# Kernel tuning notes

Hardware: AMD Instinct MI355X
Metric: run time of the kernel (lower is better)

The kernel has to match this reference:

```python
import jax, jax.numpy as jnp
import numpy as np

D_MODEL = 1024
H = 16
D_K = D_MODEL // H
D_FF = 4096
EPS = 1e-6
NEG = -1.0e9


def setup_inputs() -> dict:
    key = jax.random.key(0)
    ks = jax.random.split(key, 8)
    B, S = 4, 2048
    x = jax.random.normal(ks[0], (B, S, D_MODEL), dtype=jnp.float32)
    src_mask = jnp.ones((B, 1, S, S), dtype=jnp.int32)
    s = 0.02
    wq = jax.random.normal(ks[1], (D_MODEL, D_MODEL), jnp.float32) * s
    wk = jax.random.normal(ks[2], (D_MODEL, D_MODEL), jnp.float32) * s
    wv = jax.random.normal(ks[3], (D_MODEL, D_MODEL), jnp.float32) * s
    wo = jax.random.normal(ks[4], (D_MODEL, D_MODEL), jnp.float32) * s
    w1 = jax.random.normal(ks[5], (D_MODEL, D_FF), jnp.float32) * s
    b1 = jnp.zeros((D_FF,), jnp.float32)
    w2 = jax.random.normal(ks[6], (D_FF, D_MODEL), jnp.float32) * s
    b2 = jnp.zeros((D_MODEL,), jnp.float32)
    # LayerNorm params are scalars in the original (torch.ones(1)/zeros(1))
    a1 = jnp.ones((1,), jnp.float32); bt1 = jnp.zeros((1,), jnp.float32)
    a2 = jnp.ones((1,), jnp.float32); bt2 = jnp.zeros((1,), jnp.float32)
    return {"x": x, "src_mask": src_mask, "wq": wq, "wk": wk, "wv": wv,
            "wo": wo, "w1": w1, "b1": b1, "w2": w2, "b2": b2,
            "a1": a1, "bt1": bt1, "a2": a2, "bt2": bt2}


def _layernorm(x, alpha, beta):
    # Original: (x - mean) / (std + eps), std with Bessel correction (torch default)
    mean = jnp.mean(x, axis=-1, keepdims=True)
    std = jnp.std(x, axis=-1, keepdims=True, ddof=1)
    return alpha * (x - mean) / (std + EPS) + beta


def _mha(x, mask, wq, wk, wv, wo):
    B, S, _ = x.shape
    q = (x @ wq).reshape(B, S, H, D_K).transpose(0, 2, 1, 3)  # [B,H,S,Dk]
    k = (x @ wk).reshape(B, S, H, D_K).transpose(0, 2, 1, 3)
    v = (x @ wv).reshape(B, S, H, D_K).transpose(0, 2, 1, 3)
    scores = jnp.einsum('bhqd,bhkd->bhqk', q, k) / jnp.sqrt(jnp.float32(D_K))
    scores = jnp.where(mask == 0, NEG, scores)
    attn = jax.nn.softmax(scores, axis=-1)
    out = jnp.einsum('bhqk,bhkd->bhqd', attn, v)  # [B,H,S,Dk]
    out = out.transpose(0, 2, 1, 3).reshape(B, S, D_MODEL)
    return out @ wo


def reference(x, src_mask, wq, wk, wv, wo, w1, b1, w2, b2, a1, bt1, a2, bt2):
    # Sublayer 1: self-attention with post-norm residual (dropout = eval/identity)
    attn_out = _mha(x, src_mask, wq, wk, wv, wo)
    x = _layernorm(x + attn_out, a1, bt1)
    # Sublayer 2: FFN with post-norm residual
    ffn_out = jax.nn.relu(x @ w1 + b1) @ w2 + b2
    x = _layernorm(x + ffn_out, a2, bt2)
    return x
```

## Files before the change

kernel.cpp:

```cpp
#include <hip/hip_runtime.h>
#include <stdint.h>

typedef __bf16 bf16x8 __attribute__((ext_vector_type(8)));
typedef float f32x4 __attribute__((ext_vector_type(4)));
typedef unsigned short u16;
typedef u16 u16x8 __attribute__((ext_vector_type(8)));
typedef u16 u16x4 __attribute__((ext_vector_type(4)));
typedef uint32_t u32;

#define DEV __device__ __forceinline__

static constexpr int B_ = 4, S_ = 2048, M_ = 8192, D_ = 1024, H_ = 16, DFF_ = 4096;

DEV u16 f2bf(float f) {
    union { float f; u32 u; } c; c.f = f;
    u32 u = c.u;
    return (u16)((u + 0x7fffu + ((u >> 16) & 1u)) >> 16);
}

DEV u32 cvt_pk_bf16(float lo, float hi) {
    u32 r;
    asm("v_cvt_pk_bf16_f32 %0, %1, %2" : "=v"(r) : "v"(lo), "v"(hi));
    return r;
}

DEV float v_exp2(float x) {
    float r;
    asm("v_exp_f32 %0, %1" : "=v"(r) : "v"(x));
    return r;
}

DEV void gload16(void* lds, const void* g) {
    __builtin_amdgcn_global_load_lds(
        (const __attribute__((address_space(1))) unsigned int*)g,
        (__attribute__((address_space(3))) unsigned int*)lds, 16, 0, 0);
}


__global__ __launch_bounds__(256) void k_pack_mask(const int* __restrict__ m,
                                                   u32* __restrict__ bits, int nwords) {
    int w = blockIdx.x * 256 + threadIdx.x;
    if (w >= nwords) return;
    const int4* s = (const int4*)(m + (size_t)w * 32);
    u32 r = 0;
#pragma unroll
    for (int j = 0; j < 8; j++) {
        int4 v = s[j];
        r |= (u32)(v.x != 0) << (j * 4) | (u32)(v.y != 0) << (j * 4 + 1) |
             (u32)(v.z != 0) << (j * 4 + 2) | (u32)(v.w != 0) << (j * 4 + 3);
    }
    bits[w] = r;
}

__global__ __launch_bounds__(256) void k_cast_bf16(const float* __restrict__ s,
                                                   u16* __restrict__ d, int n4) {
    int i = blockIdx.x * 256 + threadIdx.x;
    if (i >= n4) return;
    f32x4 v = ((const f32x4*)s)[i];
    u16x4 o;
    o[0] = f2bf(v[0]); o[1] = f2bf(v[1]); o[2] = f2bf(v[2]); o[3] = f2bf(v[3]);
    ((u16x4*)d)[i] = o;
}

__global__ void k_transpose_cast(const float* __restrict__ s, u16* __restrict__ d,
                                 int K, int N) {
    __shared__ float t[32][33];
    int n0 = blockIdx.x * 32, k0 = blockIdx.y * 32;
    int tx = threadIdx.x, ty = threadIdx.y;
#pragma unroll
    for (int i = 0; i < 4; i++)
        t[ty + i * 8][tx] = s[(size_t)(k0 + ty + i * 8) * N + n0 + tx];
    __syncthreads();
#pragma unroll
    for (int i = 0; i < 4; i++)
        d[(size_t)(n0 + ty + i * 8) * K + k0 + tx] = f2bf(t[tx][ty + i * 8]);
}

__global__ __launch_bounds__(256) void k_transpose_v(const u16* __restrict__ qkv,
                                                     u16* __restrict__ vT) {
    __shared__ u16 t[64][68];
    const int bh = blockIdx.y, s0 = blockIdx.x * 64;
    const int r = threadIdx.x >> 2, c = (threadIdx.x & 3) * 16;
    const u16* src = qkv + ((size_t)(128 + bh) * 2048 + s0 + r) * 64 + c;
    *(u16x8*)&t[r][c] = *(const u16x8*)src;
    *(u16x8*)&t[r][c + 8] = *(const u16x8*)(src + 8);
    __syncthreads();
    u16x8 o0, o1;
#pragma unroll
    for (int e = 0; e < 8; e++) { o0[e] = t[c + e][r]; o1[e] = t[c + 8 + e][r]; }
    u16* dst = vT + ((size_t)bh * 64 + r) * 2048 + s0 + c;
    *(u16x8*)dst = o0;
    *(u16x8*)(dst + 8) = o1;
}

template <int EPI>
__global__ __launch_bounds__(512, 4) void k_gemm8(const u16* __restrict__ A,
                                                  const u16* __restrict__ Bt,
                                                  float* __restrict__ Cf,
                                                  u16* __restrict__ Cb,
                                                  const float* __restrict__ bias,
                                                  int N, int K) {
    __shared__ u16 As[2][128 * 64];
    __shared__ u16 Bs[2][128 * 64];
    const int tid = threadIdx.x, lane = tid & 63, wave = tid >> 6;
    const int lr = lane & 15, lg = lane >> 4;
    const int wm = wave >> 1, wn = wave & 1;
    const int nbx = N >> 7;
    const int chunk = gridDim.x >> 3;
    const int id = ((int)blockIdx.x & 7) * chunk + ((int)blockIdx.x >> 3);
    const size_t row0 = (size_t)(id / nbx) * 128;
    const int col0 = (id % nbx) * 128;
    const int srow = lane >> 3;
    const int sgr = (lane & 7) ^ (srow & 7);
    const int NT = K >> 6;
    f32x4 acc[2][4] = {};

    auto stage = [&](int buf, int t) {
#pragma unroll
        for (int i = 0; i < 2; i++) {
            int c = i * 8 + wave;
            gload16((char*)&As[buf][0] + c * 1024,
                    (const char*)(A + (row0 + c * 8 + srow) * K + t * 64 + sgr * 8));
        }
#pragma unroll
        for (int i = 0; i < 2; i++) {
            int c = i * 8 + wave;
            gload16((char*)&Bs[buf][0] + c * 1024,
                    (const char*)(Bt + (size_t)(col0 + c * 8 + srow) * K + t * 64 + sgr * 8));
        }
    };

    stage(0, 0);
    for (int t = 0; t < NT; ++t) {
        const int cur = t & 1;
        if (t + 1 < NT) {
            stage(cur ^ 1, t + 1);
            asm volatile("s_waitcnt vmcnt(4)" ::: "memory");
        } else {
            asm volatile("s_waitcnt vmcnt(0)" ::: "memory");
        }
        __builtin_amdgcn_s_barrier();
        asm volatile("" ::: "memory");
        bf16x8 bF[4][2];
#pragma unroll
        for (int n = 0; n < 4; n++) {
            int r = wn * 64 + n * 16 + lr;
            int rb = r * 128, sw = (r & 7) << 4;
#pragma unroll
            for (int ks = 0; ks < 2; ks++)
                bF[n][ks] = *(const bf16x8*)((char*)&Bs[cur][0] +
                                             (rb + ((ks * 64 + lg * 16) ^ sw)));
        }
#pragma unroll
        for (int m = 0; m < 2; m++) {
            int r = wm * 32 + m * 16 + lr;
            int rb = r * 128, sw = (r & 7) << 4;
            bf16x8 a0 = *(const bf16x8*)((char*)&As[cur][0] + (rb + ((lg * 16) ^ sw)));
            bf16x8 a1 = *(const bf16x8*)((char*)&As[cur][0] + (rb + ((64 + lg * 16) ^ sw)));
            __builtin_amdgcn_s_setprio(1);
#pragma unroll
            for (int n = 0; n < 4; n++) {
                acc[m][n] = __builtin_amdgcn_mfma_f32_16x16x32_bf16(a0, bF[n][0],
                                                                    acc[m][n], 0, 0, 0);
                acc[m][n] = __builtin_amdgcn_mfma_f32_16x16x32_bf16(a1, bF[n][1],
                                                                    acc[m][n], 0, 0, 0);
            }
            __builtin_amdgcn_s_setprio(0);
        }
        asm volatile("" ::: "memory");
        __builtin_amdgcn_s_barrier();
    }
#pragma unroll
    for (int m = 0; m < 2; m++)
#pragma unroll
        for (int n = 0; n < 4; n++)
#pragma unroll
            for (int i = 0; i < 4; i++) {
                int rg = (int)row0 + wm * 32 + m * 16 + lg * 4 + i;
                int cg = col0 + wn * 64 + n * 16 + lr;
                float v = acc[m][n][i];
                if constexpr (EPI == 0) {
                    if (cg < 1024) v *= 0.1803368801111832f;
                    int proj = cg >> 10, hh = (cg >> 6) & 15, dk = cg & 63;
                    int b = rg >> 11, s = rg & 2047;
                    size_t idx = ((size_t)(proj * 64 + b * 16 + hh) * 2048 + s) * 64 + dk;
                    Cb[idx] = f2bf(v);
                } else if constexpr (EPI == 1) {
                    Cf[(size_t)rg * N + cg] = v;
                } else if constexpr (EPI == 2) {
                    v += bias[cg];
                    v = v > 0.f ? v : 0.f;
                    Cb[(size_t)rg * N + cg] = f2bf(v);
                } else {
                    Cf[(size_t)rg * N + cg] = v + bias[cg];
                }
            }
}

__global__ __launch_bounds__(256) void k_attn(const u16* __restrict__ qkv,
                                              const u16* __restrict__ vT,
                                              const u32* __restrict__ mbits,
                                              u16* __restrict__ outb) {
    __shared__ u16 Kt[64 * 64];
    __shared__ u16 Vt[64 * 64];
    __shared__ u16 Pt[4][32 * 64];
    __shared__ u32 pm[128][2];
    const int tid = threadIdx.x, lane = tid & 63, wave = tid >> 6;
    const int lr = lane & 15, lg = lane >> 4;
    const int id0 = blockIdx.y * 16 + blockIdx.x;
    const int id = (id0 & 7) * 128 + (id0 >> 3);
    const int bh = id >> 4;
    const int b = bh >> 4, h = bh & 15;
    const int qb0 = (id & 15) * 128;
    const size_t qbase = (size_t)bh * (2048 * 64);
    const size_t kbase = (size_t)(64 + bh) * (2048 * 64);
    const size_t vtbase = (size_t)bh * (64 * 2048);

    bf16x8 qf[2][2];
    const int q0 = qb0 + wave * 32;
#pragma unroll
    for (int rs = 0; rs < 2; rs++)
#pragma unroll
        for (int kf = 0; kf < 2; kf++)
            qf[rs][kf] = *(const bf16x8*)(qkv + qbase +
                                          (size_t)(q0 + rs * 16 + lr) * 64 + kf * 32 + lg * 8);

    u16x8 ones_u;
#pragma unroll
    for (int e = 0; e < 8; e++) ones_u[e] = 0x3f80;
    const bf16x8 ones8 = *(const bf16x8*)&ones_u;

    f32x4 o[2][4] = {};
    f32x4 lacc[2] = {};
    const int str = tid >> 2, sq = tid & 3;
    const int swzs = (str & 7) << 4;
    const f32x4 zinit = {-16.f, -16.f, -16.f, -16.f};

    for (int kv0 = 0; kv0 < 2048; kv0 += 64) {
        __syncthreads();
        {
            const u16* src = qkv + kbase + (size_t)(kv0 + str) * 64 + sq * 16;
            u16x8 v0 = *(const u16x8*)src, v1 = *(const u16x8*)(src + 8);
            int b0 = str * 128 + sq * 32;
            *(u16x8*)((char*)Kt + ((b0) ^ swzs)) = v0;
            *(u16x8*)((char*)Kt + ((b0 + 16) ^ swzs)) = v1;
        }
        {
            const u16* src = vT + vtbase + (size_t)str * 2048 + kv0 + sq * 16;
            u16x8 v0 = *(const u16x8*)src, v1 = *(const u16x8*)(src + 8);
            int b0 = str * 128 + sq * 32;
            *(u16x8*)((char*)Vt + ((b0) ^ swzs)) = v0;
            *(u16x8*)((char*)Vt + ((b0 + 16) ^ swzs)) = v1;
        }
        int ql = tid >> 1, wsel = tid & 1;
        u32 mword = mbits[(size_t)(b * 2048 + qb0 + ql) * 64 + (kv0 >> 5) + wsel];
        pm[ql][wsel] = mword;
        bool allones = (__ballot(mword == 0xffffffffu) == ~0ull);
        __syncthreads();

        f32x4 st[2][4];
#pragma unroll
        for (int ks = 0; ks < 4; ks++) {
            int rr = ks * 16 + lr;
            int rb = rr * 128, sw = (rr & 7) << 4;
            bf16x8 k0 = *(const bf16x8*)((char*)Kt + ((rb + lg * 16) ^ sw));
            bf16x8 k1 = *(const bf16x8*)((char*)Kt + ((rb + 64 + lg * 16) ^ sw));
#pragma unroll
            for (int rs = 0; rs < 2; rs++) {
                f32x4 z = __builtin_amdgcn_mfma_f32_16x16x32_bf16(k0, qf[rs][0],
                                                                  zinit, 0, 0, 0);
                z = __builtin_amdgcn_mfma_f32_16x16x32_bf16(k1, qf[rs][1], z, 0, 0, 0);
                st[rs][ks] = z;
            }
        }
        if (!allones) {
#pragma unroll
            for (int rs = 0; rs < 2; rs++) {
                u32 w0 = pm[wave * 32 + rs * 16 + lr][0];
                u32 w1 = pm[wave * 32 + rs * 16 + lr][1];
#pragma unroll
                for (int ks = 0; ks < 4; ks++)
#pragma unroll
                    for (int i = 0; i < 4; i++) {
                        int kv = ks * 16 + lg * 4 + i;
                        u32 w = (kv & 32) ? w1 : w0;
                        if (!((w >> (kv & 31)) & 1u)) st[rs][ks][i] = -1e9f;
                    }
            }
        }
#pragma unroll
        for (int rs = 0; rs < 2; rs++) {
            int prow = rs * 16 + lr;
            int pb = prow * 128, swp = (prow & 7) << 4;
#pragma unroll
            for (int ks = 0; ks < 4; ks++) {
                uint2 w;
                w.x = cvt_pk_bf16(v_exp2(st[rs][ks][0]), v_exp2(st[rs][ks][1]));
                w.y = cvt_pk_bf16(v_exp2(st[rs][ks][2]), v_exp2(st[rs][ks][3]));
                *(uint2*)((char*)&Pt[wave][0] + ((pb + ks * 32 + lg * 8) ^ swp)) = w;
            }
        }
        asm volatile("s_waitcnt lgkmcnt(0)" ::: "memory");
        bf16x8 pf[2][2];
#pragma unroll
        for (int rs = 0; rs < 2; rs++) {
            int prow = rs * 16 + lr;
            int pb = prow * 128, swp = (prow & 7) << 4;
            pf[rs][0] = *(const bf16x8*)((char*)&Pt[wave][0] + ((pb + lg * 16) ^ swp));
            pf[rs][1] = *(const bf16x8*)((char*)&Pt[wave][0] + ((pb + 64 + lg * 16) ^ swp));
        }
#pragma unroll
        for (int rs = 0; rs < 2; rs++) {
            lacc[rs] = __builtin_amdgcn_mfma_f32_16x16x32_bf16(ones8, pf[rs][0],
                                                               lacc[rs], 0, 0, 0);
            lacc[rs] = __builtin_amdgcn_mfma_f32_16x16x32_bf16(ones8, pf[rs][1],
                                                               lacc[rs], 0, 0, 0);
        }
#pragma unroll
        for (int ns = 0; ns < 4; ns++) {
            int vr = ns * 16 + lr;
            int vb = vr * 128, sw = (vr & 7) << 4;
            bf16x8 v0 = *(const bf16x8*)((char*)Vt + ((vb + lg * 16) ^ sw));
            bf16x8 v1 = *(const bf16x8*)((char*)Vt + ((vb + 64 + lg * 16) ^ sw));
#pragma unroll
            for (int rs = 0; rs < 2; rs++) {
                o[rs][ns] = __builtin_amdgcn_mfma_f32_16x16x32_bf16(v0, pf[rs][0],
                                                                    o[rs][ns], 0, 0, 0);
                o[rs][ns] = __builtin_amdgcn_mfma_f32_16x16x32_bf16(v1, pf[rs][1],
                                                                    o[rs][ns], 0, 0, 0);
            }
        }
    }
#pragma unroll
    for (int rs = 0; rs < 2; rs++) {
        float inv = 1.f / lacc[rs][0];
        int qg = qb0 + wave * 32 + rs * 16 + lr;
#pragma unroll
        for (int ns = 0; ns < 4; ns++) {
            u16x4 ov;
#pragma unroll
            for (int i = 0; i < 4; i++) ov[i] = f2bf(o[rs][ns][i] * inv);
            *(u16x4*)(outb + (size_t)(b * 2048 + qg) * 1024 + h * 64 + ns * 16 + lg * 4) = ov;
        }
    }
}

template <bool WB>
__global__ __launch_bounds__(256) void k_add_ln(const float* __restrict__ y,
                                                const float* __restrict__ resid,
                                                float* __restrict__ outf,
                                                u16* __restrict__ outb,
                                                const float* __restrict__ alpha,
                                                const float* __restrict__ beta) {
    const int row = blockIdx.x, tid = threadIdx.x;
    const f32x4 a = ((const f32x4*)(y + (size_t)row * 1024))[tid];
    const f32x4 r = ((const f32x4*)(resid + (size_t)row * 1024))[tid];
    f32x4 t;
#pragma unroll
    for (int i = 0; i < 4; i++) t[i] = a[i] + r[i];
    float s = t[0] + t[1] + t[2] + t[3];
    float ss = t[0] * t[0] + t[1] * t[1] + t[2] * t[2] + t[3] * t[3];
#pragma unroll
    for (int m2 = 1; m2 < 64; m2 <<= 1) {
        s += __shfl_xor(s, m2);
        ss += __shfl_xor(ss, m2);
    }
    __shared__ float ps[4], pss[4];
    if ((tid & 63) == 0) { ps[tid >> 6] = s; pss[tid >> 6] = ss; }
    __syncthreads();
    s = ps[0] + ps[1] + ps[2] + ps[3];
    ss = pss[0] + pss[1] + pss[2] + pss[3];
    const float mean = s * (1.f / 1024.f);
    float var = (ss - 1024.f * mean * mean) * (1.f / 1023.f);
    var = fmaxf(var, 0.f);
    const float inv = alpha[0] / (sqrtf(var) + 1e-6f);
    const float bet = beta[0];
    f32x4 oo;
#pragma unroll
    for (int i = 0; i < 4; i++) oo[i] = (t[i] - mean) * inv + bet;
    ((f32x4*)(outf + (size_t)row * 1024))[tid] = oo;
    if constexpr (WB) {
        u16x4 ob;
#pragma unroll
        for (int i = 0; i < 4; i++) ob[i] = f2bf(oo[i]);
        ((u16x4*)(outb + (size_t)row * 1024))[tid] = ob;
    }
}

extern "C" void kernel_launch(void* const* d_in, const int* in_sizes, int n_in,
                              void* d_out, int out_size, void* d_ws, size_t ws_size,
                              hipStream_t stream) {
    const float* x   = (const float*)d_in[0];
    const int*   msk = (const int*)d_in[1];
    const float* wq  = (const float*)d_in[2];
    const float* wk  = (const float*)d_in[3];
    const float* wv  = (const float*)d_in[4];
    const float* wo  = (const float*)d_in[5];
    const float* w1  = (const float*)d_in[6];
    const float* b1  = (const float*)d_in[7];
    const float* w2  = (const float*)d_in[8];
    const float* b2  = (const float*)d_in[9];
    const float* a1  = (const float*)d_in[10];
    const float* bt1 = (const float*)d_in[11];
    const float* a2  = (const float*)d_in[12];
    const float* bt2 = (const float*)d_in[13];
    float* out = (float*)d_out;

    char* ws = (char*)d_ws;
    size_t off = 0;
    auto alloc = [&](size_t bytes) {
        void* p = ws + off;
        off += (bytes + 255) & ~(size_t)255;
        return p;
    };
    u16* xb    = (u16*)alloc((size_t)M_ * D_ * 2);
    u16* wqkvT = (u16*)alloc((size_t)3 * D_ * D_ * 2);
    u16* woT   = (u16*)alloc((size_t)D_ * D_ * 2);
    u16* w1T   = (u16*)alloc((size_t)DFF_ * D_ * 2);
    u16* w2T   = (u16*)alloc((size_t)D_ * DFF_ * 2);
    u32* mbits = (u32*)alloc((size_t)B_ * S_ * 64 * 4);
    u16* aout  = (u16*)alloc((size_t)M_ * D_ * 2);
    float* y   = (float*)alloc((size_t)M_ * D_ * 4);
    float* x1  = (float*)alloc((size_t)M_ * D_ * 4);
    u16* x1b   = (u16*)alloc((size_t)M_ * D_ * 2);
    u16* vTb   = (u16*)alloc((size_t)64 * 64 * 2048 * 2);
    u16* qkv   = (u16*)alloc((size_t)M_ * DFF_ * 2);
    u16* hft   = qkv;

    k_pack_mask<<<dim3((B_ * S_ * 64) / 256), 256, 0, stream>>>(msk, mbits, B_ * S_ * 64);
    k_cast_bf16<<<dim3((M_ * D_ / 4) / 256), 256, 0, stream>>>(x, xb, M_ * D_ / 4);
    dim3 tb(32, 8);
    k_transpose_cast<<<dim3(32, 32), tb, 0, stream>>>(wq, wqkvT, D_, D_);
    k_transpose_cast<<<dim3(32, 32), tb, 0, stream>>>(wk, wqkvT + D_ * D_, D_, D_);
    k_transpose_cast<<<dim3(32, 32), tb, 0, stream>>>(wv, wqkvT + 2 * D_ * D_, D_, D_);
    k_transpose_cast<<<dim3(32, 32), tb, 0, stream>>>(wo, woT, D_, D_);
    k_transpose_cast<<<dim3(128, 32), tb, 0, stream>>>(w1, w1T, D_, DFF_);
    k_transpose_cast<<<dim3(32, 128), tb, 0, stream>>>(w2, w2T, DFF_, D_);

    k_gemm8<0><<<dim3(1536), 512, 0, stream>>>(xb, wqkvT, nullptr, qkv, nullptr,
                                               3 * D_, D_);
    k_transpose_v<<<dim3(32, 64), 256, 0, stream>>>(qkv, vTb);
    k_attn<<<dim3(16, 64), 256, 0, stream>>>(qkv, vTb, mbits, aout);
    k_gemm8<1><<<dim3(512), 512, 0, stream>>>(aout, woT, y, nullptr, nullptr, D_, D_);
    k_add_ln<true><<<dim3(M_), 256, 0, stream>>>(y, x, x1, x1b, a1, bt1);
    k_gemm8<2><<<dim3(2048), 512, 0, stream>>>(x1b, w1T, nullptr, hft, b1, DFF_, D_);
    k_gemm8<3><<<dim3(512), 512, 0, stream>>>(hft, w2T, y, nullptr, b2, D_, DFF_);
    k_add_ln<false><<<dim3(M_), 256, 0, stream>>>(y, x1, out, nullptr, a2, bt2);
}
```

Baseline: 442.7 us.

## Add 256x256-tile pipelined GEMM for QKV/FFN1 and double-buffer attention K/V tiles

```diff
diff --git a/kernel.cpp b/kernel.cpp
--- a/kernel.cpp
+++ b/kernel.cpp
@@ -9,6 +9,7 @@
 typedef uint32_t u32;
 
 #define DEV __device__ __forceinline__
+#define MFMA(a, b, c) __builtin_amdgcn_mfma_f32_16x16x32_bf16(a, b, c, 0, 0, 0)
 
 static constexpr int B_ = 4, S_ = 2048, M_ = 8192, D_ = 1024, H_ = 16, DFF_ = 4096;
 
@@ -91,6 +92,153 @@
     u16* dst = vT + ((size_t)bh * 64 + r) * 2048 + s0 + c;
     *(u16x8*)dst = o0;
     *(u16x8*)(dst + 8) = o1;
+}
+
+template <int EPI>
+__global__ __launch_bounds__(512, 2) void k_gemm256(const u16* __restrict__ A,
+                                                    const u16* __restrict__ Bt,
+                                                    float* __restrict__ Cf,
+                                                    u16* __restrict__ Cb,
+                                                    const float* __restrict__ bias,
+                                                    int N, int K) {
+    __shared__ u16 As[2][256 * 64];
+    __shared__ u16 Bs[2][256 * 64];
+    const int tid = threadIdx.x, lane = tid & 63, wave = tid >> 6;
+    const int lr = lane & 15, lg = lane >> 4;
+    const int wm = wave >> 2, wn = wave & 3;
+    const int nbx = N >> 8;
+    const int chunk = gridDim.x >> 3;
+    const int id = ((int)blockIdx.x & 7) * chunk + ((int)blockIdx.x >> 3);
+    const size_t row0 = (size_t)(id / nbx) * 256;
+    const int col0 = (id % nbx) * 256;
+    const int srow = lane >> 3;
+    const int sgr = (lane & 7) ^ srow;
+    const int NT = K >> 6;
+    f32x4 acc[8][4] = {};
+
+    auto stage_half = [&](int isB, int buf, int t, int h) {
+        const u16* g = isB ? Bt : A;
+        const size_t grow0 = isB ? (size_t)col0 : row0;
+        char* base = isB ? (char*)&Bs[buf][0] : (char*)&As[buf][0];
+#pragma unroll
+        for (int l = 0; l < 2; l++) {
+            int rt = h * 128 + l * 64 + wave * 8;
+            gload16(base + rt * 128,
+                    (const char*)(g + (grow0 + rt + srow) * K + t * 64 + sgr * 8));
+        }
+    };
+    auto rdA = [&](int cur, int mh, int m, int kk) -> bf16x8 {
+        int r = wm * 128 + mh * 64 + m * 16 + lr;
+        int gi = kk * 4 + lg;
+        return *(const bf16x8*)((char*)&As[cur][0] + r * 128 + ((gi ^ (r & 7)) << 4));
+    };
+    auto rdB = [&](int cur, int nh, int n, int kk) -> bf16x8 {
+        int r = wn * 64 + nh * 32 + n * 16 + lr;
+        int gi = kk * 4 + lg;
+        return *(const bf16x8*)((char*)&Bs[cur][0] + r * 128 + ((gi ^ (r & 7)) << 4));
+    };
+
+    stage_half(0, 0, 0, 0); stage_half(0, 0, 0, 1);
+    stage_half(1, 0, 0, 0); stage_half(1, 0, 0, 1);
+    stage_half(1, 1, 1, 0); stage_half(1, 1, 1, 1);
+    asm volatile("s_waitcnt vmcnt(4)" ::: "memory");
+    __builtin_amdgcn_s_barrier();
+
+    bf16x8 aF[4][2], b0F[2][2], b1F[2][2];
+    for (int t = 0; t < NT; ++t) {
+        const int cur = t & 1, nxt = cur ^ 1;
+#pragma unroll
+        for (int m = 0; m < 4; m++) { aF[m][0] = rdA(cur, 0, m, 0); aF[m][1] = rdA(cur, 0, m, 1); }
+#pragma unroll
+        for (int n = 0; n < 2; n++) { b0F[n][0] = rdB(cur, 0, n, 0); b0F[n][1] = rdB(cur, 0, n, 1); }
+        if (t + 1 < NT) stage_half(0, nxt, t + 1, 0);
+        __builtin_amdgcn_s_barrier();
+        asm volatile("s_waitcnt lgkmcnt(0)" ::: "memory");
+        __builtin_amdgcn_sched_barrier(0);
+        __builtin_amdgcn_s_setprio(1);
+#pragma unroll
+        for (int m = 0; m < 4; m++)
+#pragma unroll
+            for (int n = 0; n < 2; n++) {
+                acc[m][n] = MFMA(aF[m][0], b0F[n][0], acc[m][n]);
+                acc[m][n] = MFMA(aF[m][1], b0F[n][1], acc[m][n]);
+            }
+        __builtin_amdgcn_s_setprio(0);
+        __builtin_amdgcn_s_barrier();
+#pragma unroll
+        for (int n = 0; n < 2; n++) { b1F[n][0] = rdB(cur, 1, n, 0); b1F[n][1] = rdB(cur, 1, n, 1); }
+        if (t + 1 < NT) stage_half(0, nxt, t + 1, 1);
+        __builtin_amdgcn_s_barrier();
+        asm volatile("s_waitcnt lgkmcnt(0)" ::: "memory");
+        __builtin_amdgcn_sched_barrier(0);
+        __builtin_amdgcn_s_setprio(1);
+#pragma unroll
+        for (int m = 0; m < 4; m++)
+#pragma unroll
+            for (int n = 0; n < 2; n++) {
+                acc[m][2 + n] = MFMA(aF[m][0], b1F[n][0], acc[m][2 + n]);
+                acc[m][2 + n] = MFMA(aF[m][1], b1F[n][1], acc[m][2 + n]);
+            }
+        __builtin_amdgcn_s_setprio(0);
+        __builtin_amdgcn_s_barrier();
+#pragma unroll
+        for (int m = 0; m < 4; m++) { aF[m][0] = rdA(cur, 1, m, 0); aF[m][1] = rdA(cur, 1, m, 1); }
+        if (t + 2 < NT) stage_half(1, cur, t + 2, 0);
+        __builtin_amdgcn_s_barrier();
+        asm volatile("s_waitcnt lgkmcnt(0)" ::: "memory");
+        __builtin_amdgcn_sched_barrier(0);
+        __builtin_amdgcn_s_setprio(1);
+#pragma unroll
+        for (int m = 0; m < 4; m++)
+#pragma unroll
+            for (int n = 0; n < 2; n++) {
+                acc[4 + m][2 + n] = MFMA(aF[m][0], b1F[n][0], acc[4 + m][2 + n]);
+                acc[4 + m][2 + n] = MFMA(aF[m][1], b1F[n][1], acc[4 + m][2 + n]);
+            }
+        __builtin_amdgcn_s_setprio(0);
+        __builtin_amdgcn_s_barrier();
+        if (t + 2 < NT) stage_half(1, cur, t + 2, 1);
+        if (t + 1 < NT) {
+            if (t + 2 < NT) asm volatile("s_waitcnt vmcnt(4)" ::: "memory");
+            else            asm volatile("s_waitcnt vmcnt(0)" ::: "memory");
+        }
+        __builtin_amdgcn_s_barrier();
+        __builtin_amdgcn_s_setprio(1);
+#pragma unroll
+        for (int m = 0; m < 4; m++)
+#pragma unroll
+            for (int n = 0; n < 2; n++) {
+                acc[4 + m][n] = MFMA(aF[m][0], b0F[n][0], acc[4 + m][n]);
+                acc[4 + m][n] = MFMA(aF[m][1], b0F[n][1], acc[4 + m][n]);
+            }
+        __builtin_amdgcn_s_setprio(0);
+        __builtin_amdgcn_s_barrier();
+    }
+#pragma unroll
+    for (int m = 0; m < 8; m++)
+#pragma unroll
+        for (int n = 0; n < 4; n++)
+#pragma unroll
+            for (int i = 0; i < 4; i++) {
+                int rg = (int)row0 + wm * 128 + m * 16 + lg * 4 + i;
+                int cg = col0 + wn * 64 + n * 16 + lr;
+                float v = acc[m][n][i];
+                if constexpr (EPI == 0) {
+                    if (cg < 1024) v *= 0.1803368801111832f;
+                    int proj = cg >> 10, hh = (cg >> 6) & 15, dk = cg & 63;
+                    int b = rg >> 11, s = rg & 2047;
+                    size_t idx = ((size_t)(proj * 64 + b * 16 + hh) * 2048 + s) * 64 + dk;
+                    Cb[idx] = f2bf(v);
+                } else if constexpr (EPI == 1) {
+                    Cf[(size_t)rg * N + cg] = v;
+                } else if constexpr (EPI == 2) {
+                    v += bias[cg];
+                    v = v > 0.f ? v : 0.f;
+                    Cb[(size_t)rg * N + cg] = f2bf(v);
+                } else {
+                    Cf[(size_t)rg * N + cg] = v + bias[cg];
+                }
+            }
 }
 
 template <int EPI>
@@ -111,7 +259,7 @@
     const size_t row0 = (size_t)(id / nbx) * 128;
     const int col0 = (id % nbx) * 128;
     const int srow = lane >> 3;
-    const int sgr = (lane & 7) ^ (srow & 7);
+    const int sgr = (lane & 7) ^ srow;
     const int NT = K >> 6;
     f32x4 acc[2][4] = {};
 
@@ -160,10 +308,8 @@
             __builtin_amdgcn_s_setprio(1);
 #pragma unroll
             for (int n = 0; n < 4; n++) {
-                acc[m][n] = __builtin_amdgcn_mfma_f32_16x16x32_bf16(a0, bF[n][0],
-                                                                    acc[m][n], 0, 0, 0);
-                acc[m][n] = __builtin_amdgcn_mfma_f32_16x16x32_bf16(a1, bF[n][1],
-                                                                    acc[m][n], 0, 0, 0);
+                acc[m][n] = MFMA(a0, bF[n][0], acc[m][n]);
+                acc[m][n] = MFMA(a1, bF[n][1], acc[m][n]);
             }
             __builtin_amdgcn_s_setprio(0);
         }
@@ -201,10 +347,10 @@
                                               const u16* __restrict__ vT,
                                               const u32* __restrict__ mbits,
                                               u16* __restrict__ outb) {
-    __shared__ u16 Kt[64 * 64];
-    __shared__ u16 Vt[64 * 64];
+    __shared__ u16 Kt[2][64 * 64];
+    __shared__ u16 Vt[2][64 * 64];
     __shared__ u16 Pt[4][32 * 64];
-    __shared__ u32 pm[128][2];
+    __shared__ u32 pm[2][128][2];
     const int tid = threadIdx.x, lane = tid & 63, wave = tid >> 6;
     const int lr = lane & 15, lg = lane >> 4;
     const int id0 = blockIdx.y * 16 + blockIdx.x;
@@ -236,48 +382,55 @@
     const int swzs = (str & 7) << 4;
     const f32x4 zinit = {-16.f, -16.f, -16.f, -16.f};
 
-    for (int kv0 = 0; kv0 < 2048; kv0 += 64) {
-        __syncthreads();
-        {
-            const u16* src = qkv + kbase + (size_t)(kv0 + str) * 64 + sq * 16;
-            u16x8 v0 = *(const u16x8*)src, v1 = *(const u16x8*)(src + 8);
-            int b0 = str * 128 + sq * 32;
-            *(u16x8*)((char*)Kt + ((b0) ^ swzs)) = v0;
-            *(u16x8*)((char*)Kt + ((b0 + 16) ^ swzs)) = v1;
-        }
-        {
-            const u16* src = vT + vtbase + (size_t)str * 2048 + kv0 + sq * 16;
-            u16x8 v0 = *(const u16x8*)src, v1 = *(const u16x8*)(src + 8);
-            int b0 = str * 128 + sq * 32;
-            *(u16x8*)((char*)Vt + ((b0) ^ swzs)) = v0;
-            *(u16x8*)((char*)Vt + ((b0 + 16) ^ swzs)) = v1;
-        }
-        int ql = tid >> 1, wsel = tid & 1;
-        u32 mword = mbits[(size_t)(b * 2048 + qb0 + ql) * 64 + (kv0 >> 5) + wsel];
-        pm[ql][wsel] = mword;
-        bool allones = (__ballot(mword == 0xffffffffu) == ~0ull);
-        __syncthreads();
+    u16x8 krA, krB, vrA, vrB; u32 mwA;
+    auto issue_loads = [&](int kv0n) {
+        const u16* ksrc = qkv + kbase + (size_t)(kv0n + str) * 64 + sq * 16;
+        krA = *(const u16x8*)ksrc; krB = *(const u16x8*)(ksrc + 8);
+        const u16* vsrc = vT + vtbase + (size_t)str * 2048 + kv0n + sq * 16;
+        vrA = *(const u16x8*)vsrc; vrB = *(const u16x8*)(vsrc + 8);
+        mwA = mbits[(size_t)(b * 2048 + qb0 + (tid >> 1)) * 64 + (kv0n >> 5) + (tid & 1)];
+    };
+    auto write_tile = [&](int buf) -> bool {
+        int b0 = str * 128 + sq * 32;
+        *(u16x8*)((char*)&Kt[buf][0] + ((b0) ^ swzs)) = krA;
+        *(u16x8*)((char*)&Kt[buf][0] + ((b0 + 16) ^ swzs)) = krB;
+        *(u16x8*)((char*)&Vt[buf][0] + ((b0) ^ swzs)) = vrA;
+        *(u16x8*)((char*)&Vt[buf][0] + ((b0 + 16) ^ swzs)) = vrB;
+        pm[buf][tid >> 1][tid & 1] = mwA;
+        return (__ballot(mwA == 0xffffffffu) == ~0ull);
+    };
+
+    issue_loads(0);
+    bool aon_nxt = write_tile(0);
+    for (int t = 0; t < 32; ++t) {
+        const int cur = t & 1;
+        const bool aon = aon_nxt ||
+                         false;
+        bool aon_cur = aon_nxt;
+        if (t + 1 < 32) issue_loads((t + 1) * 64);
+        asm volatile("s_waitcnt lgkmcnt(0)" ::: "memory");
+        __builtin_amdgcn_s_barrier();
+        (void)aon;
 
         f32x4 st[2][4];
 #pragma unroll
         for (int ks = 0; ks < 4; ks++) {
             int rr = ks * 16 + lr;
             int rb = rr * 128, sw = (rr & 7) << 4;
-            bf16x8 k0 = *(const bf16x8*)((char*)Kt + ((rb + lg * 16) ^ sw));
-            bf16x8 k1 = *(const bf16x8*)((char*)Kt + ((rb + 64 + lg * 16) ^ sw));
+            bf16x8 k0 = *(const bf16x8*)((char*)&Kt[cur][0] + ((rb + lg * 16) ^ sw));
+            bf16x8 k1 = *(const bf16x8*)((char*)&Kt[cur][0] + ((rb + 64 + lg * 16) ^ sw));
 #pragma unroll
             for (int rs = 0; rs < 2; rs++) {
-                f32x4 z = __builtin_amdgcn_mfma_f32_16x16x32_bf16(k0, qf[rs][0],
-                                                                  zinit, 0, 0, 0);
-                z = __builtin_amdgcn_mfma_f32_16x16x32_bf16(k1, qf[rs][1], z, 0, 0, 0);
+                f32x4 z = MFMA(k0, qf[rs][0], zinit);
+                z = MFMA(k1, qf[rs][1], z);
                 st[rs][ks] = z;
             }
         }
-        if (!allones) {
+        if (!aon_cur) {
 #pragma unroll
             for (int rs = 0; rs < 2; rs++) {
-                u32 w0 = pm[wave * 32 + rs * 16 + lr][0];
-                u32 w1 = pm[wave * 32 + rs * 16 + lr][1];
+                u32 w0 = pm[cur][wave * 32 + rs * 16 + lr][0];
+                u32 w1 = pm[cur][wave * 32 + rs * 16 + lr][1];
 #pragma unroll
                 for (int ks = 0; ks < 4; ks++)
 #pragma unroll
@@ -301,6 +454,7 @@
             }
         }
         asm volatile("s_waitcnt lgkmcnt(0)" ::: "memory");
+        __builtin_amdgcn_sched_barrier(0);
         bf16x8 pf[2][2];
 #pragma unroll
         for (int rs = 0; rs < 2; rs++) {
@@ -311,25 +465,22 @@
         }
 #pragma unroll
         for (int rs = 0; rs < 2; rs++) {
-            lacc[rs] = __builtin_amdgcn_mfma_f32_16x16x32_bf16(ones8, pf[rs][0],
-                                                               lacc[rs], 0, 0, 0);
-            lacc[rs] = __builtin_amdgcn_mfma_f32_16x16x32_bf16(ones8, pf[rs][1],
-                                                               lacc[rs], 0, 0, 0);
+            lacc[rs] = MFMA(ones8, pf[rs][0], lacc[rs]);
+            lacc[rs] = MFMA(ones8, pf[rs][1], lacc[rs]);
         }
 #pragma unroll
         for (int ns = 0; ns < 4; ns++) {
             int vr = ns * 16 + lr;
             int vb = vr * 128, sw = (vr & 7) << 4;
-            bf16x8 v0 = *(const bf16x8*)((char*)Vt + ((vb + lg * 16) ^ sw));
-            bf16x8 v1 = *(const bf16x8*)((char*)Vt + ((vb + 64 + lg * 16) ^ sw));
+            bf16x8 v0 = *(const bf16x8*)((char*)&Vt[cur][0] + ((vb + lg * 16) ^ sw));
+            bf16x8 v1 = *(const bf16x8*)((char*)&Vt[cur][0] + ((vb + 64 + lg * 16) ^ sw));
 #pragma unroll
             for (int rs = 0; rs < 2; rs++) {
-                o[rs][ns] = __builtin_amdgcn_mfma_f32_16x16x32_bf16(v0, pf[rs][0],
-                                                                    o[rs][ns], 0, 0, 0);
-                o[rs][ns] = __builtin_amdgcn_mfma_f32_16x16x32_bf16(v1, pf[rs][1],
-                                                                    o[rs][ns], 0, 0, 0);
-            }
-        }
+                o[rs][ns] = MFMA(v0, pf[rs][0], o[rs][ns]);
+                o[rs][ns] = MFMA(v1, pf[rs][1], o[rs][ns]);
+            }
+        }
+        if (t + 1 < 32) aon_nxt = write_tile(cur ^ 1);
     }
 #pragma unroll
     for (int rs = 0; rs < 2; rs++) {
@@ -437,13 +588,13 @@
     k_transpose_cast<<<dim3(128, 32), tb, 0, stream>>>(w1, w1T, D_, DFF_);
     k_transpose_cast<<<dim3(32, 128), tb, 0, stream>>>(w2, w2T, DFF_, D_);
 
-    k_gemm8<0><<<dim3(1536), 512, 0, stream>>>(xb, wqkvT, nullptr, qkv, nullptr,
-                                               3 * D_, D_);
+    k_gemm256<0><<<dim3(384), 512, 0, stream>>>(xb, wqkvT, nullptr, qkv, nullptr,
+                                                3 * D_, D_);
     k_transpose_v<<<dim3(32, 64), 256, 0, stream>>>(qkv, vTb);
     k_attn<<<dim3(16, 64), 256, 0, stream>>>(qkv, vTb, mbits, aout);
     k_gemm8<1><<<dim3(512), 512, 0, stream>>>(aout, woT, y, nullptr, nullptr, D_, D_);
     k_add_ln<true><<<dim3(M_), 256, 0, stream>>>(y, x, x1, x1b, a1, bt1);
-    k_gemm8<2><<<dim3(2048), 512, 0, stream>>>(x1b, w1T, nullptr, hft, b1, DFF_, D_);
+    k_gemm256<2><<<dim3(512), 512, 0, stream>>>(x1b, w1T, nullptr, hft, b1, DFF_, D_);
     k_gemm8<3><<<dim3(512), 512, 0, stream>>>(hft, w2T, y, nullptr, b2, D_, DFF_);
     k_add_ln<false><<<dim3(M_), 256, 0, stream>>>(y, x1, out, nullptr, a2, bt2);
 }
```

After: 420.1 us. -5.1%, faster.
